# Kernel optimization log

Measured on AMD Instinct MI355X. Metric: run time of the kernel, lower is better.

The kernel has to match this reference:

```python
import jax, jax.numpy as jnp
import numpy as np

B, NDOC, L, E = 32, 4, 512, 512
SCALE = np.float32(1.0 / np.sqrt(E))
NEG_INF = np.float32(-1e9)


def setup_inputs() -> dict:
    key = jax.random.key(0)
    k1, k2, k3, k4, k5, k6 = jax.random.split(key, 6)
    return {
        "x1": jax.random.normal(k1, (B, L, E), dtype=jnp.float32),
        "x2": jax.random.normal(k2, (B, NDOC, L, E), dtype=jnp.float32),
        "x1_len": jax.random.randint(k3, (B,), 0, L, dtype=jnp.int64),
        "x2_len": jax.random.randint(k4, (B, NDOC), 0, L, dtype=jnp.int64),
        "fusion_w": jax.random.normal(k5, (2 * E, E), dtype=jnp.float32) * 0.02,
        "fusion_b": jnp.zeros((E,), dtype=jnp.float32),
        "out_w": jax.random.normal(k6, (8 * E, 2 * E), dtype=jnp.float32) * 0.02,
        "out_b": jnp.zeros((2 * E,), dtype=jnp.float32),
    }


def reference(x1, x2, x1_len, x2_len, fusion_w, fusion_b, out_w, out_b):
    # Faithful to torch .repeat(1,4,...): concatenate 4 full copies along batch,
    # so attention row i pairs x1[i % B] with x2[i // 4, i % 4].
    x1_rep = jnp.tile(x1, (NDOC, 1, 1))          # [4B, L, E]
    x2_r = x2.reshape(-1, L, E)                  # [4B, L, E]

    x1_len_r = jnp.tile(x1_len, NDOC)            # [4B] (same tiling as x1_rep)
    x2_len_r = x2_len.reshape(-1)                # [4B]
    pos = jnp.arange(L)
    q_mask = pos[None, :] < x1_len_r[:, None]    # [4B, L]
    k_mask = pos[None, :] < x2_len_r[:, None]    # [4B, L]
    mask = q_mask[:, :, None] & k_mask[:, None, :]  # [4B, L, L]

    # scaled-dot-product attention with masked_fill(mask==0, -1e9)
    scores = jnp.einsum('bqe,bke->bqk', x1_rep, x2_r) * SCALE  # [4B, L, L]
    scores = jnp.where(mask, scores, NEG_INF)
    attn = jax.nn.softmax(scores, axis=-1)
    x1_att = jnp.einsum('bqk,bke->bqe', attn, x2_r)            # [4B, L, E]

    cat = jnp.concatenate([x1_rep - x1_att, x1_rep * x1_att], axis=-1)  # [4B, L, 2E]
    fus = jax.nn.relu(cat @ fusion_w + fusion_b)                        # [4B, L, E]

    x1_mean = jnp.mean(fus, axis=1)              # [4B, E]
    x1_max = jnp.max(fus, axis=1)                # [4B, E]
    pooled = jnp.concatenate([x1_mean.reshape(B, -1), x1_max.reshape(B, -1)], axis=-1)  # [B, 8E]
    out = jax.nn.relu(pooled @ out_w + out_b)    # [B, 2E]
    return out, attn
```

## Files before the change

### kernel.cpp

```cpp
#include <hip/hip_runtime.h>
#include <cstddef>

#define BATCH 32
#define NB    128
#define LL    512
#define EE    512
#define SCALE 0.044194173824159216f
#define NEG_INF -1e9f

typedef __attribute__((ext_vector_type(4))) float f32x4;
typedef __attribute__((ext_vector_type(8))) short s16x8;
typedef __attribute__((ext_vector_type(4))) unsigned short u16x4;

#define STEP_FENCE() asm volatile("s_waitcnt vmcnt(0) lgkmcnt(0)\n\ts_barrier" ::: "memory")

__device__ __forceinline__ unsigned short f2b(float f) {
    unsigned u = __float_as_uint(f);
    u += 0x7FFFu + ((u >> 16) & 1u);
    return (unsigned short)(u >> 16);
}
__device__ __forceinline__ float b2f(unsigned short h) {
    return __uint_as_float(((unsigned)h) << 16);
}

__device__ __forceinline__ void gld_lds16(const unsigned short* g, unsigned short* l) {
    __builtin_amdgcn_global_load_lds(
        (const __attribute__((address_space(1))) void*)g,
        (__attribute__((address_space(3))) void*)l, 16, 0, 0);
}

__global__ __launch_bounds__(256) void k_cvt_x1(
    const float* __restrict__ x1, unsigned short* __restrict__ x1bf)
{
    const size_t idx = (size_t)blockIdx.x * 256 + threadIdx.x;
    f32x4 v = *(const f32x4*)(x1 + idx * 4);
    u16x4 o = { f2b(v[0]), f2b(v[1]), f2b(v[2]), f2b(v[3]) };
    *(u16x4*)(x1bf + idx * 4) = o;
}

__global__ __launch_bounds__(256) void k_cvt_x2(
    const float* __restrict__ x2,
    unsigned short* __restrict__ x2bf, unsigned short* __restrict__ x2t)
{
    __shared__ float T[64][65];
    const int i = blockIdx.z, kb = blockIdx.y * 64, eb = blockIdx.x * 64;
    const float* src = x2 + (size_t)i * LL * EE;
    unsigned short* db = x2bf + (size_t)i * LL * EE;
    unsigned short* dt = x2t  + (size_t)i * LL * EE;
    const int t = threadIdx.x, r16 = t >> 4, c4 = (t & 15) * 4;
#pragma unroll
    for (int p = 0; p < 4; ++p) {
        int row = p * 16 + r16;
        f32x4 v = *(const f32x4*)(src + (size_t)(kb + row) * EE + eb + c4);
        T[row][c4] = v[0]; T[row][c4+1] = v[1]; T[row][c4+2] = v[2]; T[row][c4+3] = v[3];
        u16x4 o = { f2b(v[0]), f2b(v[1]), f2b(v[2]), f2b(v[3]) };
        *(u16x4*)(db + (size_t)(kb + row) * EE + eb + c4) = o;
    }
    __syncthreads();
#pragma unroll
    for (int p = 0; p < 4; ++p) {
        int erow = p * 16 + r16;
        u16x4 o = { f2b(T[c4][erow]), f2b(T[c4+1][erow]),
                    f2b(T[c4+2][erow]), f2b(T[c4+3][erow]) };
        *(u16x4*)(dt + (size_t)(eb + erow) * LL + kb + c4) = o;
    }
}

__global__ __launch_bounds__(256) void k_cvt_fw(
    const float* __restrict__ fw, unsigned short* __restrict__ fwt)
{
    __shared__ float T[64][65];
    const int jb = blockIdx.y * 64, eb = blockIdx.x * 64;
    const int t = threadIdx.x, r16 = t >> 4, c4 = (t & 15) * 4;
#pragma unroll
    for (int p = 0; p < 4; ++p) {
        int row = p * 16 + r16;
        f32x4 v = *(const f32x4*)(fw + (size_t)(jb + row) * EE + eb + c4);
        T[row][c4] = v[0]; T[row][c4+1] = v[1]; T[row][c4+2] = v[2]; T[row][c4+3] = v[3];
    }
    __syncthreads();
#pragma unroll
    for (int p = 0; p < 4; ++p) {
        int erow = p * 16 + r16;
#pragma unroll
        for (int k = 0; k < 4; ++k) {
            int jold = jb + c4 + k;
            int jn = (jold < 512) ? (2 * jold) : (2 * (jold - 512) + 1);
            fwt[(size_t)(eb + erow) * 1024 + jn] = f2b(T[c4 + k][erow]);
        }
    }
}

__global__ __launch_bounds__(1024, 4) void k_attn(
    const unsigned short* __restrict__ x1bf,
    const unsigned short* __restrict__ x2bf,
    const unsigned short* __restrict__ x2t,
    const int* __restrict__ x1_len, const int* __restrict__ x2_len,
    float* __restrict__ attn, unsigned short* __restrict__ Cbuf)
{
    __shared__ __align__(16) char smem[163840];
    float* rowred = (float*)(smem + 131072);
    float* rowst  = (float*)(smem + 131072 + 4096);
    unsigned short* Vst0 = (unsigned short*)(smem + 131072);
    unsigned short* Vst1 = (unsigned short*)(smem + 147456);

    const int flat = blockIdx.x + blockIdx.y * 128;
    const int xcd  = flat & 7;
    const int idx  = flat >> 3;
    const int i    = xcd * 16 + (idx >> 2);
    const int q0   = (idx & 3) * 128;
    const unsigned short* Ag = x1bf + (size_t)(i & 31) * LL * EE;
    const unsigned short* Bg = x2bf + (size_t)i * LL * EE;
    const unsigned short* Vg = x2t  + (size_t)i * LL * EE;
    const int t = threadIdx.x, lane = t & 63;
    const int w = t >> 6;
    const int m = lane & 15, quad = lane >> 4;
    const int lrow = lane >> 2, lcol = (lane & 3) * 8;
    const int wrow = w >> 3, wcol = w & 7;

    f32x4 acc[4][4];
#pragma unroll
    for (int r = 0; r < 4; ++r)
#pragma unroll
        for (int c = 0; c < 4; ++c) acc[r][c] = (f32x4){0.f, 0.f, 0.f, 0.f};

#define STAGE_SCORES(sl, base)                                                          \
    do {                                                                                \
        unsigned short* An_ = (unsigned short*)(base);                                  \
        unsigned short* Bn_ = (unsigned short*)((char*)(base) + 8192);                  \
        const int e0_ = (sl) * 32;                                                      \
        if (w < 8)                                                                      \
            gld_lds16(Ag + (size_t)(q0 + w * 16 + lrow) * EE + e0_ + lcol, &An_[w * 512]); \
        gld_lds16(Bg + (size_t)((2 * w) * 16 + lrow) * EE + e0_ + lcol, &Bn_[(2 * w) * 512]); \
        gld_lds16(Bg + (size_t)((2 * w + 1) * 16 + lrow) * EE + e0_ + lcol, &Bn_[(2 * w + 1) * 512]); \
    } while (0)

    STAGE_SCORES(0, smem);
    STAGE_SCORES(1, smem + 40960);

#pragma unroll
    for (int it = 0; it < 16; ++it) {
        if (it == 15)   asm volatile("s_waitcnt vmcnt(0)" ::: "memory");
        else if (w < 8) asm volatile("s_waitcnt vmcnt(3)" ::: "memory");
        else            asm volatile("s_waitcnt vmcnt(2)" ::: "memory");
        __builtin_amdgcn_s_barrier();
        if (it < 14) STAGE_SCORES(it + 2, smem + 40960 * ((it + 2) % 3));
        char* cb = smem + 40960 * (it % 3);
        unsigned short* Ac = (unsigned short*)cb;
        unsigned short* Bc = (unsigned short*)(cb + 8192);
        s16x8 af[4], bfr[4];
#pragma unroll
        for (int rt = 0; rt < 4; ++rt)
            af[rt] = *(const s16x8*)&Ac[(wrow * 64 + rt * 16 + m) * 32 + quad * 8];
#pragma unroll
        for (int ct = 0; ct < 4; ++ct)
            bfr[ct] = *(const s16x8*)&Bc[(wcol * 64 + ct * 16 + m) * 32 + quad * 8];
#pragma unroll
        for (int rt = 0; rt < 4; ++rt)
#pragma unroll
            for (int ct = 0; ct < 4; ++ct)
                acc[rt][ct] = __builtin_amdgcn_mfma_f32_16x16x32_bf16(
                    af[rt], bfr[ct], acc[rt][ct], 0, 0, 0);
    }
    __syncthreads();

    const int qlen = x1_len[i & 31];
    const int klen = x2_len[i];

#pragma unroll
    for (int rt = 0; rt < 4; ++rt)
#pragma unroll
        for (int reg = 0; reg < 4; ++reg) {
            const int l = q0 + wrow * 64 + rt * 16 + quad * 4 + reg;
            const bool qok = l < qlen;
#pragma unroll
            for (int ct = 0; ct < 4; ++ct) {
                const int k = wcol * 64 + ct * 16 + m;
                acc[rt][ct][reg] = (qok && k < klen) ? acc[rt][ct][reg] * SCALE : NEG_INF;
            }
        }

#pragma unroll
    for (int rt = 0; rt < 4; ++rt)
#pragma unroll
        for (int reg = 0; reg < 4; ++reg) {
            float v = fmaxf(fmaxf(acc[rt][0][reg], acc[rt][1][reg]),
                            fmaxf(acc[rt][2][reg], acc[rt][3][reg]));
            v = fmaxf(v, __shfl_xor(v, 1));
            v = fmaxf(v, __shfl_xor(v, 2));
            v = fmaxf(v, __shfl_xor(v, 4));
            v = fmaxf(v, __shfl_xor(v, 8));
            if (m == 0)
                rowred[wcol * 128 + wrow * 64 + rt * 16 + quad * 4 + reg] = v;
        }
    __syncthreads();
    if (t < 128) {
        float mx = rowred[t];
#pragma unroll
        for (int c = 1; c < 8; ++c) mx = fmaxf(mx, rowred[c * 128 + t]);
        rowst[t] = mx;
    }
    __syncthreads();

#pragma unroll
    for (int rt = 0; rt < 4; ++rt)
#pragma unroll
        for (int reg = 0; reg < 4; ++reg) {
            const int lloc = wrow * 64 + rt * 16 + quad * 4 + reg;
            const float mx = rowst[lloc];
            float s = 0.f;
#pragma unroll
            for (int ct = 0; ct < 4; ++ct) {
                float p = __expf(acc[rt][ct][reg] - mx);
                acc[rt][ct][reg] = p;
                s += p;
            }
            s += __shfl_xor(s, 1);
            s += __shfl_xor(s, 2);
            s += __shfl_xor(s, 4);
            s += __shfl_xor(s, 8);
            if (m == 0) rowred[wcol * 128 + lloc] = s;
        }
    __syncthreads();
    if (t < 128) {
        float s = 0.f;
#pragma unroll
        for (int c = 0; c < 8; ++c) s += rowred[c * 128 + t];
        rowst[t] = 1.0f / s;
    }
    __syncthreads();

    float* op = attn + (size_t)i * LL * LL;
#pragma unroll
    for (int rt = 0; rt < 4; ++rt)
#pragma unroll
        for (int reg = 0; reg < 4; ++reg) {
            const int lloc = wrow * 64 + rt * 16 + quad * 4 + reg;
            const float inv = rowst[lloc];
#pragma unroll
            for (int ct = 0; ct < 4; ++ct) {
                const int k = wcol * 64 + ct * 16 + m;
                float p = acc[rt][ct][reg] * inv;
                op[(size_t)(q0 + lloc) * LL + k] = p;
                unsigned off = (unsigned)(lloc * 1024 + k * 2) ^ (unsigned)((lloc & 7) << 4);
                *(unsigned short*)(smem + off) = f2b(p);
            }
        }
    __syncthreads();

    const int pwr = w >> 2, pwc = w & 3;
    unsigned short* Cb = Cbuf + (size_t)i * LL * 1024;
#pragma unroll
    for (int eh = 0; eh < 2; ++eh) {
        f32x4 acc2[2][4];
#pragma unroll
        for (int r = 0; r < 2; ++r)
#pragma unroll
            for (int c = 0; c < 4; ++c) acc2[r][c] = (f32x4){0.f, 0.f, 0.f, 0.f};

        gld_lds16(Vg + (size_t)(eh * 256 + w * 16 + lrow) * LL + lcol, &Vst0[w * 512]);
        STEP_FENCE();

        for (int kt = 0; kt < 16; ++kt) {
            const int k0 = kt * 32;
            unsigned short* Vc = (kt & 1) ? Vst1 : Vst0;
            if (kt < 15) {
                unsigned short* Vn = (kt & 1) ? Vst0 : Vst1;
                gld_lds16(Vg + (size_t)(eh * 256 + w * 16 + lrow) * LL + k0 + 32 + lcol,
                          &Vn[w * 512]);
            }
            s16x8 paf[2], pbf[4];
#pragma unroll
            for (int rt = 0; rt < 2; ++rt) {
                const int lr = pwr * 32 + rt * 16 + m;
                unsigned off = (unsigned)(lr * 1024 + (k0 + quad * 8) * 2)
                               ^ (unsigned)((lr & 7) << 4);
                paf[rt] = *(const s16x8*)(smem + off);
            }
#pragma unroll
            for (int ct = 0; ct < 4; ++ct)
                pbf[ct] = *(const s16x8*)&Vc[(pwc * 64 + ct * 16 + m) * 32 + quad * 8];
#pragma unroll
            for (int rt = 0; rt < 2; ++rt)
#pragma unroll
                for (int ct = 0; ct < 4; ++ct)
                    acc2[rt][ct] = __builtin_amdgcn_mfma_f32_16x16x32_bf16(
                        paf[rt], pbf[ct], acc2[rt][ct], 0, 0, 0);
            STEP_FENCE();
        }

#pragma unroll
        for (int rt = 0; rt < 2; ++rt)
#pragma unroll
            for (int reg = 0; reg < 4; ++reg) {
                const int l = q0 + pwr * 32 + rt * 16 + quad * 4 + reg;
#pragma unroll
                for (int ct = 0; ct < 4; ++ct) {
                    const int e = eh * 256 + pwc * 64 + ct * 16 + m;
                    float att = acc2[rt][ct][reg];
                    float xv  = b2f(Ag[(size_t)l * EE + e]);
                    unsigned pr = (unsigned)f2b(xv - att) | ((unsigned)f2b(xv * att) << 16);
                    *(unsigned*)(Cb + (size_t)l * 1024 + 2 * e) = pr;
                }
            }
    }
#undef STAGE_SCORES
}

__global__ __launch_bounds__(256) void k_fuse_mfma(
    const unsigned short* __restrict__ Cbuf,
    const unsigned short* __restrict__ fwt,
    const float* __restrict__ fb,
    float* __restrict__ pmean, float* __restrict__ pmax)
{
    __shared__ __align__(16) char fsm[49152];
    __shared__ float psum[2][128];
    __shared__ float pmx[2][128];
    const int i  = blockIdx.x;
    const int lt = blockIdx.y >> 2;
    const int e0 = (blockIdx.y & 3) * 128;
    const unsigned short* Ab = Cbuf + ((size_t)i * LL + lt * 128) * 1024;
    const int t = threadIdx.x, lane = t & 63;
    const int w = t >> 6, wrow = w >> 1, wcol = w & 1;
    const int m = lane & 15, quad = lane >> 4;
    const int lrow = lane >> 2, lcol = (lane & 3) * 8;

    float bias[4];
#pragma unroll
    for (int ct = 0; ct < 4; ++ct) bias[ct] = fb[e0 + wcol * 64 + ct * 16 + m];
    float csum[4] = {0.f, 0.f, 0.f, 0.f};
    float cmax[4] = {-3e38f, -3e38f, -3e38f, -3e38f};

    f32x4 acc[4][4];
#pragma unroll
    for (int r = 0; r < 4; ++r)
#pragma unroll
        for (int c = 0; c < 4; ++c) acc[r][c] = (f32x4){0.f, 0.f, 0.f, 0.f};

#define STAGE_FUSE(sl, base)                                                            \
    do {                                                                                \
        unsigned short* Al_ = (unsigned short*)(base);                                  \
        unsigned short* Bl_ = (unsigned short*)((char*)(base) + 8192);                  \
        const int j0_ = (sl) * 32;                                                      \
        _Pragma("unroll")                                                               \
        for (int c_ = 0; c_ < 2; ++c_) {                                                \
            const int s_ = c_ * 4 + w;                                                  \
            gld_lds16(Ab + (size_t)(s_ * 16 + lrow) * 1024 + j0_ + lcol, &Al_[s_ * 512]); \
            gld_lds16(fwt + (size_t)(e0 + s_ * 16 + lrow) * 1024 + j0_ + lcol, &Bl_[s_ * 512]); \
        }                                                                               \
    } while (0)

    STAGE_FUSE(0, fsm);
    STAGE_FUSE(1, fsm + 16384);

#pragma unroll
    for (int it = 0; it < 32; ++it) {
        if (it == 31) asm volatile("s_waitcnt vmcnt(0)" ::: "memory");
        else          asm volatile("s_waitcnt vmcnt(4)" ::: "memory");
        __builtin_amdgcn_s_barrier();
        if (it < 30) STAGE_FUSE(it + 2, fsm + 16384 * ((it + 2) % 3));
        char* cb = fsm + 16384 * (it % 3);
        unsigned short* Ac = (unsigned short*)cb;
        unsigned short* Bc = (unsigned short*)(cb + 8192);
        s16x8 af[4], bfr[4];
#pragma unroll
        for (int rt = 0; rt < 4; ++rt)
            af[rt] = *(const s16x8*)&Ac[(wrow * 64 + rt * 16 + m) * 32 + quad * 8];
#pragma unroll
        for (int ct = 0; ct < 4; ++ct)
            bfr[ct] = *(const s16x8*)&Bc[(wcol * 64 + ct * 16 + m) * 32 + quad * 8];
#pragma unroll
        for (int rt = 0; rt < 4; ++rt)
#pragma unroll
            for (int ct = 0; ct < 4; ++ct)
                acc[rt][ct] = __builtin_amdgcn_mfma_f32_16x16x32_bf16(
                    af[rt], bfr[ct], acc[rt][ct], 0, 0, 0);
    }
#undef STAGE_FUSE
#pragma unroll
    for (int rt = 0; rt < 4; ++rt)
#pragma unroll
        for (int reg = 0; reg < 4; ++reg)
#pragma unroll
            for (int ct = 0; ct < 4; ++ct) {
                float f = fmaxf(acc[rt][ct][reg] + bias[ct], 0.f);
                csum[ct] += f;
                cmax[ct] = fmaxf(cmax[ct], f);
            }
#pragma unroll
    for (int ct = 0; ct < 4; ++ct) {
        csum[ct] += __shfl_xor(csum[ct], 16);
        csum[ct] += __shfl_xor(csum[ct], 32);
        cmax[ct] = fmaxf(cmax[ct], __shfl_xor(cmax[ct], 16));
        cmax[ct] = fmaxf(cmax[ct], __shfl_xor(cmax[ct], 32));
    }
    if (quad == 0) {
#pragma unroll
        for (int ct = 0; ct < 4; ++ct) {
            psum[wrow][wcol * 64 + ct * 16 + m] = csum[ct];
            pmx[wrow][wcol * 64 + ct * 16 + m] = cmax[ct];
        }
    }
    __syncthreads();
    if (t < 128) {
        float s  = psum[0][t] + psum[1][t];
        float mx = fmaxf(pmx[0][t], pmx[1][t]);
        pmean[((size_t)i * 4 + lt) * EE + e0 + t] = s;
        pmax[((size_t)i * 4 + lt) * EE + e0 + t]  = mx;
    }
}

__global__ __launch_bounds__(256) void k_out_split(
    const float* __restrict__ pmean, const float* __restrict__ pmax,
    const float* __restrict__ ow, float* __restrict__ partial)
{
    __shared__ float ps[256];
    const int kc = blockIdx.x;
    const int b  = blockIdx.y;
    const int t  = threadIdx.x;
    const int j  = kc * 256 + t;
    const int jj = (j < 2048) ? j : j - 2048;
    const int ii = 4 * b + (jj >> 9);
    const int e  = jj & 511;
    float v;
    if (j < 2048) {
        const float* bp = pmean + (size_t)ii * 4 * EE + e;
        v = (bp[0] + bp[512] + bp[1024] + bp[1536]) * (1.0f / 512.0f);
    } else {
        const float* bp = pmax + (size_t)ii * 4 * EE + e;
        v = fmaxf(fmaxf(bp[0], bp[512]), fmaxf(bp[1024], bp[1536]));
    }
    ps[t] = v;
    __syncthreads();
    f32x4 acc = {0.f, 0.f, 0.f, 0.f};
    const float* wp = ow + (size_t)kc * 256 * 1024 + t * 4;
#pragma unroll 8
    for (int q = 0; q < 256; ++q) {
        f32x4 w4 = *(const f32x4*)(wp + (size_t)q * 1024);
        float p = ps[q];
        acc[0] = fmaf(p, w4[0], acc[0]);
        acc[1] = fmaf(p, w4[1], acc[1]);
        acc[2] = fmaf(p, w4[2], acc[2]);
        acc[3] = fmaf(p, w4[3], acc[3]);
    }
    *(f32x4*)(partial + ((size_t)kc * 32 + b) * 1024 + t * 4) = acc;
}

__global__ __launch_bounds__(256) void k_out_final(
    const float* __restrict__ partial, const float* __restrict__ ob,
    float* __restrict__ out)
{
    const int idx = blockIdx.x * 256 + threadIdx.x;
    const int b = idx >> 10, o = idx & 1023;
    float s = ob[o];
#pragma unroll
    for (int kc = 0; kc < 16; ++kc)
        s += partial[((size_t)kc * 32 + b) * 1024 + o];
    out[idx] = fmaxf(s, 0.f);
}

extern "C" void kernel_launch(void* const* d_in, const int* in_sizes, int n_in,
                              void* d_out, int out_size, void* d_ws, size_t ws_size,
                              hipStream_t stream)
{
    const float* x1     = (const float*)d_in[0];
    const float* x2     = (const float*)d_in[1];
    const int*   x1_len = (const int*)d_in[2];
    const int*   x2_len = (const int*)d_in[3];
    const float* fw     = (const float*)d_in[4];
    const float* fb     = (const float*)d_in[5];
    const float* ow     = (const float*)d_in[6];
    const float* ob     = (const float*)d_in[7];

    float* out  = (float*)d_out;
    float* attn = out + (size_t)BATCH * 1024;

    char* wp = (char*)d_ws;
    unsigned short* x1bf   = (unsigned short*)wp; wp += (size_t)BATCH * LL * EE * 2;
    unsigned short* x2bf   = (unsigned short*)wp; wp += (size_t)NB * LL * EE * 2;
    unsigned short* x2t    = (unsigned short*)wp; wp += (size_t)NB * LL * EE * 2;
    unsigned short* Cbuf   = (unsigned short*)wp; wp += (size_t)NB * LL * 1024 * 2;
    unsigned short* fwt    = (unsigned short*)wp; wp += (size_t)EE * 1024 * 2;
    float* pmean   = (float*)wp; wp += (size_t)NB * 4 * EE * 4;
    float* pmax    = (float*)wp; wp += (size_t)NB * 4 * EE * 4;
    float* partial = (float*)wp; wp += (size_t)16 * BATCH * 1024 * 4;

    k_cvt_x1<<<dim3(BATCH * LL * EE / 4 / 256), 256, 0, stream>>>(x1, x1bf);
    k_cvt_x2<<<dim3(8, 8, NB), 256, 0, stream>>>(x2, x2bf, x2t);
    k_cvt_fw<<<dim3(8, 16), 256, 0, stream>>>(fw, fwt);
    k_attn<<<dim3(128, 4), 1024, 0, stream>>>(x1bf, x2bf, x2t, x1_len, x2_len, attn, Cbuf);
    k_fuse_mfma<<<dim3(128, 16), 256, 0, stream>>>(Cbuf, fwt, fb, pmean, pmax);
    k_out_split<<<dim3(16, BATCH), 256, 0, stream>>>(pmean, pmax, ow, partial);
    k_out_final<<<dim3(BATCH * 1024 / 256), 256, 0, stream>>>(partial, ob, out);
}
```

Before: 548.6 us.

## Fuse fusion-layer GEMM and pooling into attention kernel, dropping Cbuf round trip

The attention kernel now keeps both halves of the attn@V result in registers, writes the concatenated (x1-att, x1*att) tile into swizzled LDS, and runs the fusion-weight GEMM plus ReLU, sum and max pooling in the same block. The separate k_fuse_mfma launch and the 128 MB bf16 Cbuf write and read go away. In exchange, register pressure rises from holding two accumulator sets plus a 4x4 GEMM accumulator. The weight loads are single-buffered, with a fence on every step, so the fused GEMM loses the triple-buffered pipelining of the old kernel.

```diff
diff --git a/kernel.cpp b/kernel.cpp
--- a/kernel.cpp
+++ b/kernel.cpp
@@ -95,20 +95,27 @@
     const unsigned short* __restrict__ x1bf,
     const unsigned short* __restrict__ x2bf,
     const unsigned short* __restrict__ x2t,
+    const unsigned short* __restrict__ fwt,
     const int* __restrict__ x1_len, const int* __restrict__ x2_len,
-    float* __restrict__ attn, unsigned short* __restrict__ Cbuf)
+    float* __restrict__ attn,
+    const float* __restrict__ fb,
+    float* __restrict__ pmean, float* __restrict__ pmax)
 {
     __shared__ __align__(16) char smem[163840];
     float* rowred = (float*)(smem + 131072);
     float* rowst  = (float*)(smem + 131072 + 4096);
     unsigned short* Vst0 = (unsigned short*)(smem + 131072);
     unsigned short* Vst1 = (unsigned short*)(smem + 147456);
+    unsigned short* Bf   = (unsigned short*)(smem + 131072);
+    float* psum2 = (float*)(smem + 131072);
+    float* pmx2  = (float*)(smem + 131072 + 4096);
 
     const int flat = blockIdx.x + blockIdx.y * 128;
     const int xcd  = flat & 7;
     const int idx  = flat >> 3;
     const int i    = xcd * 16 + (idx >> 2);
-    const int q0   = (idx & 3) * 128;
+    const int qt   = idx & 3;
+    const int q0   = qt * 128;
     const unsigned short* Ag = x1bf + (size_t)(i & 31) * LL * EE;
     const unsigned short* Bg = x2bf + (size_t)i * LL * EE;
     const unsigned short* Vg = x2t  + (size_t)i * LL * EE;
@@ -163,6 +170,7 @@
                     af[rt], bfr[ct], acc[rt][ct], 0, 0, 0);
     }
     __syncthreads();
+#undef STAGE_SCORES
 
     const int qlen = x1_len[i & 31];
     const int klen = x2_len[i];
@@ -249,14 +257,18 @@
     __syncthreads();
 
     const int pwr = w >> 2, pwc = w & 3;
-    unsigned short* Cb = Cbuf + (size_t)i * LL * 1024;
+    f32x4 acc2a[2][4], acc2b[2][4];
+#pragma unroll
+    for (int r = 0; r < 2; ++r)
+#pragma unroll
+        for (int c = 0; c < 4; ++c) {
+            acc2a[r][c] = (f32x4){0.f, 0.f, 0.f, 0.f};
+            acc2b[r][c] = (f32x4){0.f, 0.f, 0.f, 0.f};
+        }
+
 #pragma unroll
     for (int eh = 0; eh < 2; ++eh) {
-        f32x4 acc2[2][4];
-#pragma unroll
-        for (int r = 0; r < 2; ++r)
-#pragma unroll
-            for (int c = 0; c < 4; ++c) acc2[r][c] = (f32x4){0.f, 0.f, 0.f, 0.f};
+        f32x4 (*pacc)[4] = eh ? acc2b : acc2a;
 
         gld_lds16(Vg + (size_t)(eh * 256 + w * 16 + lrow) * LL + lcol, &Vst0[w * 512]);
         STEP_FENCE();
@@ -284,111 +296,80 @@
             for (int rt = 0; rt < 2; ++rt)
 #pragma unroll
                 for (int ct = 0; ct < 4; ++ct)
-                    acc2[rt][ct] = __builtin_amdgcn_mfma_f32_16x16x32_bf16(
-                        paf[rt], pbf[ct], acc2[rt][ct], 0, 0, 0);
+                    pacc[rt][ct] = __builtin_amdgcn_mfma_f32_16x16x32_bf16(
+                        paf[rt], pbf[ct], pacc[rt][ct], 0, 0, 0);
             STEP_FENCE();
         }
-
+    }
+
+    f32x4 acc3[4][4];
+#pragma unroll
+    for (int r = 0; r < 4; ++r)
+#pragma unroll
+        for (int c = 0; c < 4; ++c) acc3[r][c] = (f32x4){0.f, 0.f, 0.f, 0.f};
+
+#pragma unroll
+    for (int h = 0; h < 2; ++h) {
+        f32x4 (*pc)[4] = h ? acc2b : acc2a;
 #pragma unroll
         for (int rt = 0; rt < 2; ++rt)
 #pragma unroll
             for (int reg = 0; reg < 4; ++reg) {
-                const int l = q0 + pwr * 32 + rt * 16 + quad * 4 + reg;
+                const int l = pwr * 32 + rt * 16 + quad * 4 + reg;
 #pragma unroll
                 for (int ct = 0; ct < 4; ++ct) {
-                    const int e = eh * 256 + pwc * 64 + ct * 16 + m;
-                    float att = acc2[rt][ct][reg];
-                    float xv  = b2f(Ag[(size_t)l * EE + e]);
+                    const int el = pwc * 64 + ct * 16 + m;
+                    const int e  = h * 256 + el;
+                    float att = pc[rt][ct][reg];
+                    float xv  = b2f(Ag[(size_t)(q0 + l) * EE + e]);
                     unsigned pr = (unsigned)f2b(xv - att) | ((unsigned)f2b(xv * att) << 16);
-                    *(unsigned*)(Cb + (size_t)l * 1024 + 2 * e) = pr;
+                    unsigned off = (unsigned)(l * 1024 + el * 4) ^ (unsigned)((l & 7) << 4);
+                    *(unsigned*)(smem + off) = pr;
                 }
             }
-    }
-#undef STAGE_SCORES
-}
-
-__global__ __launch_bounds__(256) void k_fuse_mfma(
-    const unsigned short* __restrict__ Cbuf,
-    const unsigned short* __restrict__ fwt,
-    const float* __restrict__ fb,
-    float* __restrict__ pmean, float* __restrict__ pmax)
-{
-    __shared__ __align__(16) char fsm[49152];
-    __shared__ float psum[2][128];
-    __shared__ float pmx[2][128];
-    const int i  = blockIdx.x;
-    const int lt = blockIdx.y >> 2;
-    const int e0 = (blockIdx.y & 3) * 128;
-    const unsigned short* Ab = Cbuf + ((size_t)i * LL + lt * 128) * 1024;
-    const int t = threadIdx.x, lane = t & 63;
-    const int w = t >> 6, wrow = w >> 1, wcol = w & 1;
-    const int m = lane & 15, quad = lane >> 4;
-    const int lrow = lane >> 2, lcol = (lane & 3) * 8;
-
-    float bias[4];
-#pragma unroll
-    for (int ct = 0; ct < 4; ++ct) bias[ct] = fb[e0 + wcol * 64 + ct * 16 + m];
+        __syncthreads();
+
+        for (int j0 = 0; j0 < 512; j0 += 32) {
+            gld_lds16(fwt + (size_t)((2 * w) * 16 + lrow) * 1024 + h * 512 + j0 + lcol,
+                      &Bf[(2 * w) * 512]);
+            gld_lds16(fwt + (size_t)((2 * w + 1) * 16 + lrow) * 1024 + h * 512 + j0 + lcol,
+                      &Bf[(2 * w + 1) * 512]);
+            STEP_FENCE();
+            s16x8 af[4], bfr[4];
+#pragma unroll
+            for (int rt = 0; rt < 4; ++rt) {
+                const int row = wrow * 64 + rt * 16 + m;
+                unsigned off = (unsigned)(row * 1024 + (j0 + quad * 8) * 2)
+                               ^ (unsigned)((row & 7) << 4);
+                af[rt] = *(const s16x8*)(smem + off);
+            }
+#pragma unroll
+            for (int ct = 0; ct < 4; ++ct)
+                bfr[ct] = *(const s16x8*)&Bf[(wcol * 64 + ct * 16 + m) * 32 + quad * 8];
+#pragma unroll
+            for (int rt = 0; rt < 4; ++rt)
+#pragma unroll
+                for (int ct = 0; ct < 4; ++ct)
+                    acc3[rt][ct] = __builtin_amdgcn_mfma_f32_16x16x32_bf16(
+                        af[rt], bfr[ct], acc3[rt][ct], 0, 0, 0);
+            asm volatile("s_waitcnt lgkmcnt(0)" ::: "memory");
+            __builtin_amdgcn_s_barrier();
+        }
+    }
+
     float csum[4] = {0.f, 0.f, 0.f, 0.f};
     float cmax[4] = {-3e38f, -3e38f, -3e38f, -3e38f};
-
-    f32x4 acc[4][4];
-#pragma unroll
-    for (int r = 0; r < 4; ++r)
-#pragma unroll
-        for (int c = 0; c < 4; ++c) acc[r][c] = (f32x4){0.f, 0.f, 0.f, 0.f};
-
-#define STAGE_FUSE(sl, base)                                                            \
-    do {                                                                                \
-        unsigned short* Al_ = (unsigned short*)(base);                                  \
-        unsigned short* Bl_ = (unsigned short*)((char*)(base) + 8192);                  \
-        const int j0_ = (sl) * 32;                                                      \
-        _Pragma("unroll")                                                               \
-        for (int c_ = 0; c_ < 2; ++c_) {                                                \
-            const int s_ = c_ * 4 + w;                                                  \
-            gld_lds16(Ab + (size_t)(s_ * 16 + lrow) * 1024 + j0_ + lcol, &Al_[s_ * 512]); \
-            gld_lds16(fwt + (size_t)(e0 + s_ * 16 + lrow) * 1024 + j0_ + lcol, &Bl_[s_ * 512]); \
-        }                                                                               \
-    } while (0)
-
-    STAGE_FUSE(0, fsm);
-    STAGE_FUSE(1, fsm + 16384);
-
-#pragma unroll
-    for (int it = 0; it < 32; ++it) {
-        if (it == 31) asm volatile("s_waitcnt vmcnt(0)" ::: "memory");
-        else          asm volatile("s_waitcnt vmcnt(4)" ::: "memory");
-        __builtin_amdgcn_s_barrier();
-        if (it < 30) STAGE_FUSE(it + 2, fsm + 16384 * ((it + 2) % 3));
-        char* cb = fsm + 16384 * (it % 3);
-        unsigned short* Ac = (unsigned short*)cb;
-        unsigned short* Bc = (unsigned short*)(cb + 8192);
-        s16x8 af[4], bfr[4];
+#pragma unroll
+    for (int ct = 0; ct < 4; ++ct) {
+        const float bias = fb[wcol * 64 + ct * 16 + m];
 #pragma unroll
         for (int rt = 0; rt < 4; ++rt)
-            af[rt] = *(const s16x8*)&Ac[(wrow * 64 + rt * 16 + m) * 32 + quad * 8];
-#pragma unroll
-        for (int ct = 0; ct < 4; ++ct)
-            bfr[ct] = *(const s16x8*)&Bc[(wcol * 64 + ct * 16 + m) * 32 + quad * 8];
-#pragma unroll
-        for (int rt = 0; rt < 4; ++rt)
-#pragma unroll
-            for (int ct = 0; ct < 4; ++ct)
-                acc[rt][ct] = __builtin_amdgcn_mfma_f32_16x16x32_bf16(
-                    af[rt], bfr[ct], acc[rt][ct], 0, 0, 0);
-    }
-#undef STAGE_FUSE
-#pragma unroll
-    for (int rt = 0; rt < 4; ++rt)
-#pragma unroll
-        for (int reg = 0; reg < 4; ++reg)
-#pragma unroll
-            for (int ct = 0; ct < 4; ++ct) {
-                float f = fmaxf(acc[rt][ct][reg] + bias[ct], 0.f);
+#pragma unroll
+            for (int reg = 0; reg < 4; ++reg) {
+                float f = fmaxf(acc3[rt][ct][reg] + bias, 0.f);
                 csum[ct] += f;
                 cmax[ct] = fmaxf(cmax[ct], f);
             }
-#pragma unroll
-    for (int ct = 0; ct < 4; ++ct) {
         csum[ct] += __shfl_xor(csum[ct], 16);
         csum[ct] += __shfl_xor(csum[ct], 32);
         cmax[ct] = fmaxf(cmax[ct], __shfl_xor(cmax[ct], 16));
@@ -397,16 +378,16 @@
     if (quad == 0) {
 #pragma unroll
         for (int ct = 0; ct < 4; ++ct) {
-            psum[wrow][wcol * 64 + ct * 16 + m] = csum[ct];
-            pmx[wrow][wcol * 64 + ct * 16 + m] = cmax[ct];
-        }
-    }
-    __syncthreads();
-    if (t < 128) {
-        float s  = psum[0][t] + psum[1][t];
-        float mx = fmaxf(pmx[0][t], pmx[1][t]);
-        pmean[((size_t)i * 4 + lt) * EE + e0 + t] = s;
-        pmax[((size_t)i * 4 + lt) * EE + e0 + t]  = mx;
+            psum2[wrow * 512 + wcol * 64 + ct * 16 + m] = csum[ct];
+            pmx2 [wrow * 512 + wcol * 64 + ct * 16 + m] = cmax[ct];
+        }
+    }
+    __syncthreads();
+    if (t < 512) {
+        float s  = psum2[t] + psum2[512 + t];
+        float mx = fmaxf(pmx2[t], pmx2[512 + t]);
+        pmean[((size_t)i * 4 + qt) * EE + t] = s;
+        pmax [((size_t)i * 4 + qt) * EE + t] = mx;
     }
 }
 
@@ -479,7 +460,6 @@
     unsigned short* x1bf   = (unsigned short*)wp; wp += (size_t)BATCH * LL * EE * 2;
     unsigned short* x2bf   = (unsigned short*)wp; wp += (size_t)NB * LL * EE * 2;
     unsigned short* x2t    = (unsigned short*)wp; wp += (size_t)NB * LL * EE * 2;
-    unsigned short* Cbuf   = (unsigned short*)wp; wp += (size_t)NB * LL * 1024 * 2;
     unsigned short* fwt    = (unsigned short*)wp; wp += (size_t)EE * 1024 * 2;
     float* pmean   = (float*)wp; wp += (size_t)NB * 4 * EE * 4;
     float* pmax    = (float*)wp; wp += (size_t)NB * 4 * EE * 4;
@@ -488,8 +468,8 @@
     k_cvt_x1<<<dim3(BATCH * LL * EE / 4 / 256), 256, 0, stream>>>(x1, x1bf);
     k_cvt_x2<<<dim3(8, 8, NB), 256, 0, stream>>>(x2, x2bf, x2t);
     k_cvt_fw<<<dim3(8, 16), 256, 0, stream>>>(fw, fwt);
-    k_attn<<<dim3(128, 4), 1024, 0, stream>>>(x1bf, x2bf, x2t, x1_len, x2_len, attn, Cbuf);
-    k_fuse_mfma<<<dim3(128, 16), 256, 0, stream>>>(Cbuf, fwt, fb, pmean, pmax);
+    k_attn<<<dim3(128, 4), 1024, 0, stream>>>(x1bf, x2bf, x2t, fwt, x1_len, x2_len,
+                                              attn, fb, pmean, pmax);
     k_out_split<<<dim3(16, BATCH), 256, 0, stream>>>(pmean, pmax, ow, partial);
     k_out_final<<<dim3(BATCH * 1024 / 256), 256, 0, stream>>>(partial, ob, out);
 }
```

New measurement: 681.3 us. 1.24x slower.
